# Performance work log

Hardware: AMD Instinct MI355X
Metric: run time of the kernel (lower is better)

Reference implementation:

```python
import jax, jax.numpy as jnp
import numpy as np

HIDDEN = 2560
N_HEADS = 16
N_KV = 4
HEAD_DIM = 256
GQA = N_HEADS // N_KV
INNER = N_HEADS * HEAD_DIM  # 4096
B, L = 2, 2048
ROPE_THETA = 1000000.0
EPS = 1e-6


def _rope_tables(seq_len, dim, theta):
    pos = np.arange(seq_len, dtype=np.float32)
    inv_freq = 1.0 / (theta ** (np.arange(0, dim, 2, dtype=np.float32) / dim))
    ang = pos[:, None] * inv_freq[None, :]          # [L, dim/2]
    ang = np.concatenate([ang, ang], axis=-1)        # [L, dim]
    return jnp.asarray(np.cos(ang)), jnp.asarray(np.sin(ang))


def setup_inputs() -> dict:
    key = jax.random.key(0)
    ks = jax.random.split(key, 6)
    hidden_states = jax.random.normal(ks[0], (B, L, HIDDEN), dtype=jnp.float32)
    cos, sin = _rope_tables(L, HEAD_DIM, ROPE_THETA)
    s = 0.02
    Wq = jax.random.normal(ks[1], (HIDDEN, 2 * INNER), dtype=jnp.float32) * s
    Wk = jax.random.normal(ks[2], (HIDDEN, N_KV * HEAD_DIM), dtype=jnp.float32) * s
    Wv = jax.random.normal(ks[3], (HIDDEN, N_KV * HEAD_DIM), dtype=jnp.float32) * s
    Wo = jax.random.normal(ks[4], (INNER, HIDDEN), dtype=jnp.float32) * s
    q_norm_w = jnp.ones((HEAD_DIM,), dtype=jnp.float32)
    k_norm_w = jnp.ones((HEAD_DIM,), dtype=jnp.float32)
    return {"hidden_states": hidden_states, "cos": cos, "sin": sin,
            "Wq": Wq, "Wk": Wk, "Wv": Wv, "Wo": Wo,
            "q_norm_w": q_norm_w, "k_norm_w": k_norm_w}


def _rms_norm(x, w):
    var = jnp.mean(jnp.square(x), axis=-1, keepdims=True)
    return x * jax.lax.rsqrt(var + EPS) * w


def _apply_rotary(x, cos, sin):
    # x: [B, H, L, D]; cos/sin: [L, D]
    d = x.shape[-1]
    x1, x2 = x[..., : d // 2], x[..., d // 2:]
    return x * cos + jnp.concatenate([-x2, x1], axis=-1) * sin


def reference(hidden_states, cos, sin, Wq, Wk, Wv, Wo, q_norm_w, k_norm_w):
    Bv, Lv, _ = hidden_states.shape
    qg = hidden_states @ Wq                              # [B, L, 2*INNER]
    q, gate = qg[..., :INNER], qg[..., INNER:]
    k = (hidden_states @ Wk).reshape(Bv, Lv, N_KV, HEAD_DIM)
    v = (hidden_states @ Wv).reshape(Bv, Lv, N_KV, HEAD_DIM)

    q = _rms_norm(q.reshape(Bv, Lv, N_HEADS, HEAD_DIM), q_norm_w).transpose(0, 2, 1, 3)  # [B,H,L,D]
    k = _rms_norm(k, k_norm_w).transpose(0, 2, 1, 3)     # [B,KV,L,D]
    v = v.transpose(0, 2, 1, 3)                          # [B,KV,L,D]

    q = _apply_rotary(q, cos, sin)
    k = _apply_rotary(k, cos, sin)

    # repeat_interleave over head dim for GQA
    k = jnp.repeat(k, GQA, axis=1)                       # [B,H,L,D]
    v = jnp.repeat(v, GQA, axis=1)

    scale = 1.0 / jnp.sqrt(jnp.float32(HEAD_DIM))
    scores = jnp.einsum('bhqd,bhkd->bhqk', q, k) * scale  # [B,H,L,L]
    causal = jnp.tril(jnp.ones((Lv, Lv), dtype=bool))
    scores = jnp.where(causal, scores, jnp.finfo(scores.dtype).min)
    attn = jax.nn.softmax(scores, axis=-1)
    out = jnp.einsum('bhqk,bhkd->bhqd', attn, v)          # [B,H,L,D]

    out = out.transpose(0, 2, 1, 3).reshape(Bv, Lv, INNER) * jax.nn.silu(gate)
    return out @ Wo
```

## Files before the change

kernel.cpp:

```cpp
#include <hip/hip_runtime.h>
#include <cstdint>
#include <cstddef>

#define NQKV 10240

typedef __bf16 bf16;
typedef __attribute__((ext_vector_type(4))) __bf16 bvec4;
typedef __attribute__((ext_vector_type(8))) __bf16 bvec8;
typedef __attribute__((ext_vector_type(4))) float fvec4;

__device__ __forceinline__ void gll16(const bf16* g, bf16* l) {
  __builtin_amdgcn_global_load_lds(
      (const __attribute__((address_space(1))) void*)g,
      (__attribute__((address_space(3))) void*)l, 16, 0, 0);
}

__global__ __launch_bounds__(256) void cvt_f32_bf16(const float* __restrict__ x,
                                                    bf16* __restrict__ y, int n) {
  int i = (blockIdx.x * 256 + threadIdx.x) * 4;
  if (i < n) {
    float4 v = *(const float4*)(x + i);
    bvec4 o;
    o.x = (bf16)v.x; o.y = (bf16)v.y; o.z = (bf16)v.z; o.w = (bf16)v.w;
    *(bvec4*)(y + i) = o;
  }
}

__global__ __launch_bounds__(256) void wtrans(const float* __restrict__ W,
                                              bf16* __restrict__ Wt, int K, int N) {
  __shared__ float t[64][65];
  int n0 = blockIdx.x * 64, k0 = blockIdx.y * 64;
  int tx = threadIdx.x & 63, tg = threadIdx.x >> 6;
#pragma unroll
  for (int i = 0; i < 16; ++i) {
    int r = tg * 16 + i;
    t[r][tx] = W[(size_t)(k0 + r) * N + n0 + tx];
  }
  __syncthreads();
#pragma unroll
  for (int i = 0; i < 16; ++i) {
    int r = tg * 16 + i;
    Wt[(size_t)(n0 + r) * K + k0 + tx] = (bf16)t[tx][r];
  }
}

__global__ __launch_bounds__(256) void vtrans(const bf16* __restrict__ QKV,
                                              bf16* __restrict__ Vt) {
  __shared__ bf16 t[64][65];
  int l0 = blockIdx.x * 64, dd0 = blockIdx.y * 64;
  int bkv = blockIdx.z, b = bkv >> 2, kv = bkv & 3;
  int tx = threadIdx.x & 63, tg = threadIdx.x >> 6;
#pragma unroll
  for (int i = 0; i < 16; ++i) {
    int r = tg * 16 + i;
    t[r][tx] = QKV[(size_t)(b * 2048 + l0 + r) * NQKV + 9216 + kv * 256 + dd0 + tx];
  }
  __syncthreads();
#pragma unroll
  for (int i = 0; i < 16; ++i) {
    int r = tg * 16 + i;
    Vt[((size_t)bkv * 256 + dd0 + r) * 2048 + l0 + tx] = t[tx][r];
  }
}

__global__ __launch_bounds__(256) void norm_rope(const bf16* __restrict__ QKV,
    const float* __restrict__ cosT, const float* __restrict__ sinT,
    const float* __restrict__ qw, const float* __restrict__ kw,
    bf16* __restrict__ Qn, bf16* __restrict__ Kn) {
  int u = blockIdx.x * 4 + (threadIdx.x >> 6);
  int lane = threadIdx.x & 63;
  int token = u / 20, slot = u - token * 20;
  int b = token >> 11, l = token & 2047;
  int d0 = lane * 4;
  const float* w;
  int col0;
  bf16* outp;
  if (slot < 16) {
    col0 = slot * 256; w = qw;
    outp = Qn + ((size_t)((b * 16 + slot) * 2048 + l)) * 256;
  } else {
    int kv = slot - 16;
    col0 = 8192 + kv * 256; w = kw;
    outp = Kn + ((size_t)((b * 4 + kv) * 2048 + l)) * 256;
  }
  bvec4 xi = *(const bvec4*)(QKV + (size_t)token * NQKV + col0 + d0);
  float x[4];
#pragma unroll
  for (int j = 0; j < 4; ++j) x[j] = (float)xi[j];
  float ss = x[0] * x[0] + x[1] * x[1] + x[2] * x[2] + x[3] * x[3];
#pragma unroll
  for (int off = 32; off; off >>= 1) ss += __shfl_xor(ss, off);
  float rn = rsqrtf(ss * (1.0f / 256.0f) + 1e-6f);
  float xn[4];
#pragma unroll
  for (int j = 0; j < 4; ++j) xn[j] = x[j] * rn * w[d0 + j];
  bvec4 o;
#pragma unroll
  for (int j = 0; j < 4; ++j) {
    float other = __shfl_xor(xn[j], 32);
    float rot = (lane < 32) ? -other : other;
    float c = cosT[(size_t)l * 256 + d0 + j];
    float s = sinT[(size_t)l * 256 + d0 + j];
    o[j] = (bf16)(xn[j] * c + rot * s);
  }
  *(bvec4*)(outp + d0) = o;
}

template <typename OutT>
__global__ __launch_bounds__(256, 2) void gemm8(const bf16* __restrict__ A,
                                                const bf16* __restrict__ B,
                                                OutT* __restrict__ C,
                                                int N, int Kd) {
  __shared__ alignas(16) bf16 smem[36864];
  int tid = threadIdx.x, wave = tid >> 6, lane = tid & 63;
  int quad = lane >> 4, l15 = lane & 15;
  int wm = wave >> 1, wn = wave & 1;
  int bm = blockIdx.y, bn = blockIdx.x;
  const bf16* Ag = A + (size_t)bm * 128 * Kd;
  const bf16* Bg = B + (size_t)bn * 256 * Kd;

  bf16* b0 = smem;
  bf16* b1 = smem + 12288;
  bf16* b2 = smem + 24576;

  int nt = Kd >> 5;
  int srow = lane >> 2;
  int sc8 = ((lane & 3) ^ ((lane >> 3) & 3)) * 8;
  int csw = (quad ^ ((l15 >> 1) & 3)) * 8;

  const fvec4 FZ = {0.f, 0.f, 0.f, 0.f};
  fvec4 acc[4][8];
#pragma unroll
  for (int i = 0; i < 4; ++i)
#pragma unroll
    for (int j = 0; j < 8; ++j) acc[i][j] = FZ;

  auto stage = [&](bf16* dst, int ktel) {
#pragma unroll
    for (int i = 0; i < 6; ++i) {
      int s = wave * 6 + i;
      if (s < 8) {
        gll16(Ag + (size_t)(s * 16 + srow) * Kd + ktel + sc8, dst + s * 512);
      } else {
        gll16(Bg + (size_t)((s - 8) * 16 + srow) * Kd + ktel + sc8,
              dst + 4096 + (s - 8) * 512);
      }
    }
  };

  stage(b0, 0);
  stage(b1, 32);

  for (int t = 0; t < nt; ++t) {
    asm volatile("s_waitcnt vmcnt(6)" ::: "memory");
    __builtin_amdgcn_s_barrier();
    const bf16* Ab = b0;
    const bf16* Bb = b0 + 4096;
    bvec8 af[4], bv[8];
#pragma unroll
    for (int mt = 0; mt < 4; ++mt)
      af[mt] = *(const bvec8*)(Ab + (wm * 64 + mt * 16 + l15) * 32 + csw);
#pragma unroll
    for (int nt2 = 0; nt2 < 8; ++nt2)
      bv[nt2] = *(const bvec8*)(Bb + (wn * 128 + nt2 * 16 + l15) * 32 + csw);
    int t2 = t + 2;
    if (t2 >= nt) t2 = nt - 1;
    stage(b2, t2 * 32);
    __builtin_amdgcn_s_setprio(1);
#pragma unroll
    for (int mt = 0; mt < 4; ++mt)
#pragma unroll
      for (int nt2 = 0; nt2 < 8; ++nt2)
        acc[mt][nt2] = __builtin_amdgcn_mfma_f32_16x16x32_bf16(af[mt], bv[nt2],
                                                               acc[mt][nt2], 0, 0, 0);
    __builtin_amdgcn_s_setprio(0);
    bf16* tp = b0; b0 = b1; b1 = b2; b2 = tp;
  }

#pragma unroll
  for (int mt = 0; mt < 4; ++mt)
#pragma unroll
    for (int nt2 = 0; nt2 < 8; ++nt2)
#pragma unroll
      for (int r = 0; r < 4; ++r) {
        int row = bm * 128 + wm * 64 + mt * 16 + quad * 4 + r;
        int col = bn * 256 + wn * 128 + nt2 * 16 + l15;
        C[(size_t)row * N + col] = (OutT)acc[mt][nt2][r];
      }
}

__global__ __launch_bounds__(512, 2) void flash(const bf16* __restrict__ Q,
    const bf16* __restrict__ K, const bf16* __restrict__ Vt,
    const bf16* __restrict__ QKV, bf16* __restrict__ Og) {
  __shared__ alignas(16) bf16 smem[74752];

  int lin = blockIdx.x + 8 * blockIdx.y;
  int swz = (lin & 7) * 32 + (lin >> 3);
  int pairi = swz & 7;
  int bh = swz >> 3, b = bh >> 4, h = bh & 15, kvh = (h >> 2) & 3;
  int tid = threadIdx.x, wave = tid >> 6, lane = tid & 63;
  int quad = lane >> 4, l15 = lane & 15;
  bf16* Pw = smem + 65536 + wave * 1152;

  const bf16* Qh = Q + ((size_t)(b * 16 + h) * 2048) * 256;
  const bf16* Kb = K + ((size_t)(b * 4 + kvh) * 2048) * 256;
  const bf16* Vb = Vt + ((size_t)(b * 4 + kvh) * 256) * 2048;
  const fvec4 FZ = {0.f, 0.f, 0.f, 0.f};

  auto stageKV = [&](int sel, int kt2) {
    int k0s = kt2 * 64;
    bf16* Kd = smem + sel * 16384;
    bf16* Vd = smem + 32768 + sel * 16384;
#pragma unroll
    for (int i = 0; i < 4; ++i) {
      int seg = wave * 4 + i;
      int krow = seg * 2 + (lane >> 5);
      int kc = (lane & 31) ^ (krow & 31);
      gll16(Kb + (size_t)(k0s + krow) * 256 + kc * 8, Kd + seg * 512);
      int vrow = seg * 8 + (lane >> 3);
      int vc = (lane & 7) ^ (vrow & 7);
      gll16(Vb + (size_t)vrow * 2048 + k0s + vc * 8, Vd + seg * 512);
    }
  };

  for (int half = 0; half < 2; ++half) {
    int qt = half ? (15 - pairi) : pairi;
    int q0 = qt * 128;
    int nkt = 2 * qt + 2;

    bvec8 qf[8];
    {
      int row = q0 + wave * 16 + l15;
#pragma unroll
      for (int kk = 0; kk < 8; ++kk) {
        bvec8 v = *(const bvec8*)(Qh + (size_t)row * 256 + kk * 32 + quad * 8);
#pragma unroll
        for (int j = 0; j < 8; ++j) v[j] = (bf16)((float)v[j] * 0.0625f);
        qf[kk] = v;
      }
    }

    fvec4 acc[16];
#pragma unroll
    for (int i = 0; i < 16; ++i) acc[i] = FZ;
    float m_run[4], l_run[4];
#pragma unroll
    for (int r = 0; r < 4; ++r) { m_run[r] = -3.0e38f; l_run[r] = 0.f; }

    stageKV(0, 0);
    __syncthreads();

    for (int kt = 0; kt < nkt; ++kt) {
      int cur = kt & 1;
      if (kt + 1 < nkt) stageKV(cur ^ 1, kt + 1);
      int k0 = kt * 64;
      const bf16* Ks = smem + cur * 16384;
      const bf16* Vts = smem + 32768 + cur * 16384;
      if (k0 <= q0 + wave * 16 + 15) {
        fvec4 s[4];
#pragma unroll
        for (int nt = 0; nt < 4; ++nt) {
          s[nt] = FZ;
          int row = nt * 16 + l15;
          int rm = row & 31;
          __builtin_amdgcn_s_setprio(1);
#pragma unroll
          for (int ks = 0; ks < 8; ++ks) {
            int c = ks * 4 + quad;
            bvec8 kf = *(const bvec8*)(Ks + (size_t)row * 256 + (size_t)(c ^ rm) * 8);
            s[nt] = __builtin_amdgcn_mfma_f32_16x16x32_bf16(qf[ks], kf, s[nt], 0, 0, 0);
          }
          __builtin_amdgcn_s_setprio(0);
        }

        if (k0 + 63 > q0 + wave * 16) {
#pragma unroll
          for (int nt = 0; nt < 4; ++nt)
#pragma unroll
            for (int r = 0; r < 4; ++r)
              if (k0 + nt * 16 + l15 > q0 + wave * 16 + quad * 4 + r)
                s[nt][r] = -3.0e38f;
        }

        {
          float pmax[4];
#pragma unroll
          for (int r = 0; r < 4; ++r) {
            float m = fmaxf(fmaxf(s[0][r], s[1][r]),
                            fmaxf(s[2][r], s[3][r]));
#pragma unroll
            for (int off = 8; off; off >>= 1) m = fmaxf(m, __shfl_xor(m, off));
            pmax[r] = m;
          }
          int need = 0;
#pragma unroll
          for (int r = 0; r < 4; ++r) need |= (pmax[r] > m_run[r] + 8.0f) ? 1 : 0;
          if (__any(need)) {
#pragma unroll
            for (int r = 0; r < 4; ++r) {
              float Mn = fmaxf(m_run[r], pmax[r]);
              float alpha = __expf(m_run[r] - Mn);
              m_run[r] = Mn;
              l_run[r] *= alpha;
#pragma unroll
              for (int nt = 0; nt < 16; ++nt) acc[nt][r] *= alpha;
            }
          }
          float rs[4] = {0.f, 0.f, 0.f, 0.f};
#pragma unroll
          for (int nt = 0; nt < 4; ++nt)
#pragma unroll
            for (int r = 0; r < 4; ++r) {
              float p = __expf(s[nt][r] - m_run[r]);
              rs[r] += p;
              Pw[(quad * 4 + r) * 72 + nt * 16 + l15] = (bf16)p;
            }
#pragma unroll
          for (int r = 0; r < 4; ++r) {
#pragma unroll
            for (int off = 8; off; off >>= 1) rs[r] += __shfl_xor(rs[r], off);
            l_run[r] += rs[r];
          }
        }

#pragma unroll
        for (int ks = 0; ks < 2; ++ks) {
          bvec8 pf = *(const bvec8*)(Pw + l15 * 72 + ks * 32 + quad * 8);
          __builtin_amdgcn_s_setprio(1);
#pragma unroll
          for (int nt = 0; nt < 16; ++nt) {
            int row = nt * 16 + l15;
            int c = ks * 4 + quad;
            bvec8 vf = *(const bvec8*)(Vts + (size_t)row * 64 + (size_t)(c ^ (row & 7)) * 8);
            acc[nt] = __builtin_amdgcn_mfma_f32_16x16x32_bf16(pf, vf, acc[nt], 0, 0, 0);
          }
          __builtin_amdgcn_s_setprio(0);
        }
      }
      __syncthreads();
    }

#pragma unroll
    for (int r = 0; r < 4; ++r) {
      int token = b * 2048 + q0 + wave * 16 + quad * 4 + r;
      float inv = 1.0f / l_run[r];
#pragma unroll
      for (int nt = 0; nt < 16; ++nt) {
        int col = h * 256 + nt * 16 + l15;
        float g = (float)QKV[(size_t)token * NQKV + 4096 + col];
        float silu = g / (1.0f + __expf(-g));
        Og[(size_t)token * 4096 + col] = (bf16)(acc[nt][r] * inv * silu);
      }
    }
  }
}

extern "C" void kernel_launch(void* const* d_in, const int* in_sizes, int n_in,
                              void* d_out, int out_size, void* d_ws, size_t ws_size,
                              hipStream_t stream) {
  const float* hs   = (const float*)d_in[0];
  const float* cosT = (const float*)d_in[1];
  const float* sinT = (const float*)d_in[2];
  const float* Wq   = (const float*)d_in[3];
  const float* Wk   = (const float*)d_in[4];
  const float* Wv   = (const float*)d_in[5];
  const float* Wo   = (const float*)d_in[6];
  const float* qw   = (const float*)d_in[7];
  const float* kw   = (const float*)d_in[8];
  float* out = (float*)d_out;

  char* p = (char*)d_ws;
  auto alloc = [&](size_t bytes) {
    char* r = p;
    p += (bytes + 255) & ~(size_t)255;
    return r;
  };
  bf16* Xb    = (bf16*)alloc((size_t)4096 * 2560 * 2);
  bf16* Wqkvt = (bf16*)alloc((size_t)10240 * 2560 * 2);
  bf16* Wot   = (bf16*)alloc((size_t)2560 * 4096 * 2);
  bf16* QKV   = (bf16*)alloc((size_t)4096 * 10240 * 2);
  bf16* Qn    = (bf16*)alloc((size_t)2 * 16 * 2048 * 256 * 2);
  bf16* Kn    = (bf16*)alloc((size_t)2 * 4 * 2048 * 256 * 2);
  bf16* Vtb   = (bf16*)alloc((size_t)2 * 4 * 256 * 2048 * 2);
  bf16* Og    = (bf16*)alloc((size_t)4096 * 4096 * 2);

  cvt_f32_bf16<<<10240, 256, 0, stream>>>(hs, Xb, 4096 * 2560);
  wtrans<<<dim3(128, 40), 256, 0, stream>>>(Wq, Wqkvt, 2560, 8192);
  wtrans<<<dim3(16, 40), 256, 0, stream>>>(Wk, Wqkvt + (size_t)8192 * 2560, 2560, 1024);
  wtrans<<<dim3(16, 40), 256, 0, stream>>>(Wv, Wqkvt + (size_t)9216 * 2560, 2560, 1024);
  wtrans<<<dim3(40, 64), 256, 0, stream>>>(Wo, Wot, 4096, 2560);

  gemm8<bf16><<<dim3(40, 32), 256, 0, stream>>>(Xb, Wqkvt, QKV, 10240, 2560);

  norm_rope<<<20480, 256, 0, stream>>>(QKV, cosT, sinT, qw, kw, Qn, Kn);
  vtrans<<<dim3(32, 4, 8), 256, 0, stream>>>(QKV, Vtb);

  flash<<<dim3(8, 32), 512, 0, stream>>>(Qn, Kn, Vtb, QKV, Og);

  gemm8<float><<<dim3(10, 32), 256, 0, stream>>>(Og, Wot, out, 2560, 4096);
}
```

Before: 725.6 us.

## Add 256x256-tile 8-wave GEMM with phased LDS pipeline for QKV projection

Adds a new GEMM kernel that uses 256x256 output tiles, 512 threads and a K-step of 64. It double-buffers swizzled LDS tiles and interleaves half-tile async global-to-LDS loads with MFMA phases, using setprio and explicit barriers. The QKV projection now uses this kernel in place of the 128x256 gemm8. The aim is more operand reuse per loaded byte and better overlap of loads with MFMA. The cost is 128KB of LDS per block, which limits occupancy, and a grid of only 640 blocks.

```diff
diff --git a/kernel.cpp b/kernel.cpp
--- a/kernel.cpp
+++ b/kernel.cpp
@@ -107,6 +107,113 @@
 }
 
 template <typename OutT>
+__global__ __launch_bounds__(512, 2) void gemm256(const bf16* __restrict__ A,
+                                                  const bf16* __restrict__ B,
+                                                  OutT* __restrict__ C,
+                                                  int N, int Kd) {
+  __shared__ alignas(16) bf16 smem[65536];
+  int tid = threadIdx.x, wave = tid >> 6, lane = tid & 63;
+  int quad = lane >> 4, l15 = lane & 15;
+  int wm = wave >> 2, wn = wave & 3;
+  int bn = blockIdx.x, bm = blockIdx.y;
+  const bf16* Ag = A + (size_t)bm * 256 * Kd;
+  const bf16* Bg = B + (size_t)bn * 256 * Kd;
+
+  int kx = l15 & 7;
+  int arow0 = wm * 128 + l15;
+  int brow0 = wn * 64 + l15;
+
+  const fvec4 FZ = {0.f, 0.f, 0.f, 0.f};
+  fvec4 acc[8][4];
+#pragma unroll
+  for (int i = 0; i < 8; ++i)
+#pragma unroll
+    for (int j = 0; j < 4; ++j) acc[i][j] = FZ;
+  bvec8 bq[4][2];
+
+  auto stageH = [&](int tb2, int isB, int h, int kt) {
+    const bf16* G = isB ? Bg : Ag;
+    bf16* base = smem + tb2 * 32768 + isB * 16384 + h * 8192;
+#pragma unroll
+    for (int i = 0; i < 2; ++i) {
+      int sg = wave * 2 + i;
+      int row = h * 128 + sg * 8 + (lane >> 3);
+      int c = (lane & 7) ^ ((lane >> 3) & 7);
+      gll16(G + (size_t)row * Kd + kt * 64 + c * 8, base + sg * 512);
+    }
+  };
+
+#define PH(TB, Q, LOADB, STB, SISB, SH, SKT)                                   \
+  {                                                                            \
+    const bf16* tb_ = smem + (TB) * 32768;                                     \
+    if (LOADB) {                                                               \
+      _Pragma("unroll") for (int nf = 0; nf < 4; ++nf)                         \
+        _Pragma("unroll") for (int s = 0; s < 2; ++s)                          \
+          bq[nf][s] = *(const bvec8*)(tb_ + 16384 + (brow0 + nf * 16) * 64 +   \
+                                      ((s * 4 + quad) ^ kx) * 8);              \
+    }                                                                          \
+    bvec8 af_[2][2];                                                           \
+    _Pragma("unroll") for (int mf = 0; mf < 2; ++mf)                           \
+      _Pragma("unroll") for (int s = 0; s < 2; ++s)                            \
+        af_[mf][s] = *(const bvec8*)(tb_ + (arow0 + (Q) * 32 + mf * 16) * 64 + \
+                                     ((s * 4 + quad) ^ kx) * 8);               \
+    stageH(STB, SISB, SH, SKT);                                                \
+    __builtin_amdgcn_s_barrier();                                              \
+    asm volatile("s_waitcnt lgkmcnt(0)" ::: "memory");                         \
+    __builtin_amdgcn_sched_barrier(0);                                         \
+    __builtin_amdgcn_s_setprio(1);                                             \
+    _Pragma("unroll") for (int s = 0; s < 2; ++s)                              \
+      _Pragma("unroll") for (int mf = 0; mf < 2; ++mf)                         \
+        _Pragma("unroll") for (int nf = 0; nf < 4; ++nf)                       \
+          acc[(Q) * 2 + mf][nf] = __builtin_amdgcn_mfma_f32_16x16x32_bf16(     \
+              af_[mf][s], bq[nf][s], acc[(Q) * 2 + mf][nf], 0, 0, 0);          \
+    __builtin_amdgcn_s_setprio(0);                                             \
+    if ((Q) == 3) asm volatile("s_waitcnt vmcnt(4)" ::: "memory");             \
+    __builtin_amdgcn_s_barrier();                                              \
+  }
+
+  int nt = Kd >> 6;
+  int ni = nt >> 1;
+
+  stageH(0, 1, 0, 0);
+  stageH(0, 1, 1, 0);
+  stageH(0, 0, 0, 0);
+  stageH(0, 0, 1, 0);
+  stageH(1, 1, 0, 1);
+  stageH(1, 1, 1, 1);
+  asm volatile("s_waitcnt vmcnt(4)" ::: "memory");
+  __builtin_amdgcn_s_barrier();
+
+  for (int it = 0; it < ni; ++it) {
+    int t = it * 2;
+    int tp1 = t + 1;
+    int tp2 = (t + 2 < nt) ? t + 2 : nt - 1;
+    int tp3 = (t + 3 < nt) ? t + 3 : nt - 1;
+    PH(0, 0, 1, 1, 0, 0, tp1)
+    PH(0, 1, 0, 1, 0, 1, tp1)
+    PH(0, 2, 0, 0, 1, 0, tp2)
+    PH(0, 3, 0, 0, 1, 1, tp2)
+    PH(1, 0, 1, 0, 0, 0, tp2)
+    PH(1, 1, 0, 0, 0, 1, tp2)
+    PH(1, 2, 0, 1, 1, 0, tp3)
+    PH(1, 3, 0, 1, 1, 1, tp3)
+  }
+#undef PH
+  asm volatile("s_waitcnt vmcnt(0)" ::: "memory");
+
+#pragma unroll
+  for (int am = 0; am < 8; ++am)
+#pragma unroll
+    for (int nf = 0; nf < 4; ++nf)
+#pragma unroll
+      for (int r = 0; r < 4; ++r) {
+        int row = bm * 256 + wm * 128 + am * 16 + quad * 4 + r;
+        int col = bn * 256 + wn * 64 + nf * 16 + l15;
+        C[(size_t)row * N + col] = (OutT)acc[am][nf][r];
+      }
+}
+
+template <typename OutT>
 __global__ __launch_bounds__(256, 2) void gemm8(const bf16* __restrict__ A,
                                                 const bf16* __restrict__ B,
                                                 OutT* __restrict__ C,
@@ -390,7 +497,7 @@
   wtrans<<<dim3(16, 40), 256, 0, stream>>>(Wv, Wqkvt + (size_t)9216 * 2560, 2560, 1024);
   wtrans<<<dim3(40, 64), 256, 0, stream>>>(Wo, Wot, 4096, 2560);
 
-  gemm8<bf16><<<dim3(40, 32), 256, 0, stream>>>(Xb, Wqkvt, QKV, 10240, 2560);
+  gemm256<bf16><<<dim3(40, 16), 512, 0, stream>>>(Xb, Wqkvt, QKV, 10240, 2560);
 
   norm_rope<<<20480, 256, 0, stream>>>(QKV, cosT, sinT, qw, kw, Qn, Kn);
   vtrans<<<dim3(32, 4, 8), 256, 0, stream>>>(QKV, Vtb);
```

Result: faster. 699.2 us (-3.6%).
